# Kernel tuning notes

Measured on AMD Instinct MI355X. Metric: run time of the kernel, lower is better.

Reference implementation:

```python
import jax, jax.numpy as jnp
import numpy as np

NEG_SLOPE = 0.2  # PyG GATConv default negative_slope
EPS = 1e-16      # PyG softmax denominator epsilon


def setup_inputs() -> dict:
    key = jax.random.key(0)
    N, C, H, E = 50000, 64, 12, 400000
    k = jax.random.split(key, 5)
    x = jax.random.normal(k[0], (N, C), dtype=jnp.float32)
    edge_index = jax.random.randint(k[1], (2, E), 0, N, dtype=jnp.int32)
    W = jax.random.normal(k[2], (C, H * C), dtype=jnp.float32) * (1.0 / np.sqrt(C))
    att_src = jax.random.normal(k[3], (H, C), dtype=jnp.float32) * 0.1
    att_dst = jax.random.normal(k[4], (H, C), dtype=jnp.float32) * 0.1
    bias = jnp.zeros((C,), dtype=jnp.float32)
    return {"x": x, "edge_index": edge_index, "W": W,
            "att_src": att_src, "att_dst": att_dst, "bias": bias}


def reference(x, edge_index, W, att_src, att_dst, bias):
    N, C = x.shape
    H = att_src.shape[0]
    # GATConv default add_self_loops=True
    loops = jnp.arange(N, dtype=edge_index.dtype)
    src = jnp.concatenate([edge_index[0], loops])  # message source j
    dst = jnp.concatenate([edge_index[1], loops])  # message target i

    h = (x @ W).reshape(N, H, C)                   # [N,H,C] projected features
    a_src = jnp.einsum('nhc,hc->nh', h, att_src)   # [N,H]
    a_dst = jnp.einsum('nhc,hc->nh', h, att_dst)   # [N,H]

    alpha = jax.nn.leaky_relu(a_src[src] + a_dst[dst], NEG_SLOPE)  # [E',H]
    # segment softmax over destination neighborhoods
    m = jax.ops.segment_max(alpha, dst, num_segments=N)
    alpha = jnp.exp(alpha - m[dst])
    denom = jax.ops.segment_sum(alpha, dst, num_segments=N)
    alpha = alpha / (denom[dst] + EPS)

    msg = h[src] * alpha[:, :, None]               # [E',H,C]
    out = jax.ops.segment_sum(msg, dst, num_segments=N)  # [N,H,C]
    y = out.mean(axis=1) + bias                    # concat=False -> head mean
    return jax.nn.relu(x + y)
```

## Files before the change

### kernel.cpp

```cpp
#include <hip/hip_runtime.h>
#include <hip/hip_bf16.h>


typedef __bf16 bf16x8 __attribute__((ext_vector_type(8)));
typedef float  f32x4  __attribute__((ext_vector_type(4)));
typedef float  f32x2  __attribute__((ext_vector_type(2)));

#define HEADS 12
#define CH 64
#define HC 768
#define CAP 64
#define ACOLS 24
#define ZSTRIDE 776

__device__ inline float readlane_f(float v, int lane) {
    return __builtin_bit_cast(float,
        __builtin_amdgcn_readlane(__builtin_bit_cast(int, v), lane));
}

__global__ __launch_bounds__(256) void k_pre(
    const float* __restrict__ W,
    const float* __restrict__ att_src, const float* __restrict__ att_dst,
    int* __restrict__ cnt, __bf16* __restrict__ Wt2, __bf16* __restrict__ Vt,
    int N) {
    const int nb_z = (N + 255) >> 8;
    const int nb_w = (CH * HC) >> 8;
    int b = blockIdx.x, tid = threadIdx.x;
    if (b < nb_z) {
        int i = b * 256 + tid;
        if (i < N) cnt[i] = 0;
        return;
    }
    b -= nb_z;
    if (b < nb_w) {
        int t = b * 256 + tid;
        int c = t / HC, kk = t % HC;
        int k = kk & 63;
        Wt2[t] = (__bf16)W[(size_t)k * HC + (kk - k) + c];
        return;
    }
    b -= nb_w;
    if (b >= 2 * HEADS) {
        if (tid < CH) Vt[b * CH + tid] = (__bf16)0.f;
        return;
    }
    const float* att = (b < HEADS) ? att_src + b * CH
                                   : att_dst + (b - HEADS) * CH;
    int k = tid >> 2, cq = tid & 3;
    const float* wr = W + (size_t)k * HC + (b % HEADS) * CH + cq * 16;
    float s = 0.f;
#pragma unroll
    for (int j = 0; j < 16; ++j) s += wr[j] * att[cq * 16 + j];
    s += __shfl_xor(s, 1, 64);
    s += __shfl_xor(s, 2, 64);
    if (cq == 0) Vt[b * CH + k] = (__bf16)s;
}

__global__ __launch_bounds__(256) void k_main(
    const float* __restrict__ x, const int* __restrict__ ei,
    const __bf16* __restrict__ Vt,
    int* __restrict__ cnt, int* __restrict__ adj,
    __bf16* __restrict__ xb, float* __restrict__ a_all, int N, int E) {
    const int EP = E + N;
    const int nb_build = (EP + 255) >> 8;
    int b = blockIdx.x, tid = threadIdx.x;

    if (b < nb_build) {
        int e = b * 256 + tid;
        if (e < EP) {
            int d, s;
            if (e < E) { d = ei[E + e]; s = ei[e]; }
            else       { d = e - E;     s = d; }
            int pos = atomicAdd(&cnt[d], 1);
            if (pos < CAP) adj[d * CAP + pos] = s;
        }
        return;
    }
    b -= nb_build;
    int wave = tid >> 6, lane = tid & 63;
    int m = lane & 15, quad = lane >> 4;
    int m0 = b * 64 + wave * 16;
    int row = m0 + m;
    int rc = row < N ? row : N - 1;
    const float* xa = x + (size_t)rc * CH + quad * 8;
    f32x4 v0 = *(const f32x4*)xa;
    f32x4 v1 = *(const f32x4*)(xa + 4);
    f32x4 v2 = *(const f32x4*)(xa + 32);
    f32x4 v3 = *(const f32x4*)(xa + 36);
    bf16x8 a0, a1;
#pragma unroll
    for (int j = 0; j < 4; ++j) {
        a0[j] = (__bf16)v0[j]; a0[4 + j] = (__bf16)v1[j];
        a1[j] = (__bf16)v2[j]; a1[4 + j] = (__bf16)v3[j];
    }
    if (row < N) {
        *(bf16x8*)(xb + (size_t)row * CH + quad * 8) = a0;
        *(bf16x8*)(xb + (size_t)row * CH + quad * 8 + 32) = a1;
    }
#pragma unroll
    for (int t = 0; t < 2; ++t) {
        const __bf16* bp = Vt + (size_t)(t * 16 + m) * CH + quad * 8;
        bf16x8 b0 = *(const bf16x8*)bp;
        bf16x8 b1 = *(const bf16x8*)(bp + 32);
        f32x4 acc = {0.f, 0.f, 0.f, 0.f};
        acc = __builtin_amdgcn_mfma_f32_16x16x32_bf16(a0, b0, acc, 0, 0, 0);
        acc = __builtin_amdgcn_mfma_f32_16x16x32_bf16(a1, b1, acc, 0, 0, 0);
        int col = t * 16 + m;
        if (col < ACOLS) {
#pragma unroll
            for (int r = 0; r < 4; ++r) {
                int rr = m0 + quad * 4 + r;
                if (rr < N) a_all[(size_t)rr * ACOLS + col] = acc[r];
            }
        }
    }
}

__global__ __launch_bounds__(256) void k_fused(
    const int* __restrict__ cnt, const int* __restrict__ adj,
    const float* __restrict__ a_all,
    const __bf16* __restrict__ xb, const __bf16* __restrict__ Wt2,
    const float* __restrict__ x, const float* __restrict__ bias,
    float* __restrict__ out, int N) {
    __shared__ __bf16 zt[16 * ZSTRIDE];
    int lane = threadIdx.x & 63;
    int wave = __builtin_amdgcn_readfirstlane(threadIdx.x >> 6);
    int base = blockIdx.x * 16;

    int degj[4], slj[4];
#pragma unroll
    for (int j = 0; j < 4; ++j) {
        int d = base + wave * 4 + j;
        int dg = __builtin_amdgcn_readfirstlane(cnt[d]);
        degj[j] = dg < CAP ? dg : CAP;
        int sraw = 0;
        if (lane < 32) sraw = adj[d * CAP + lane];
        slj[j] = sraw;
    }

#pragma unroll
    for (int j = 0; j < 4; ++j) {
        int row = wave * 4 + j;
        int d = base + row;
        int deg = degj[j];
        int s_l = slj[j];
        if (deg > 32 && lane >= 32)
            s_l = adj[d * CAP + lane];
        s_l = s_l < 0 ? 0 : (s_l >= N ? N - 1 : s_l);

        float adf[HEADS];
        {
            const f32x4* p = (const f32x4*)(a_all + (size_t)d * ACOLS + HEADS);
            f32x4 t0 = p[0], t1 = p[1], t2 = p[2];
#pragma unroll
            for (int u = 0; u < 4; ++u) { adf[u] = t0[u]; adf[4 + u] = t1[u]; adf[8 + u] = t2[u]; }
        }
        float w[HEADS];
        {
            const f32x4* p = (const f32x4*)(a_all + (size_t)s_l * ACOLS);
            f32x4 t0 = p[0], t1 = p[1], t2 = p[2];
            float asf[HEADS];
#pragma unroll
            for (int u = 0; u < 4; ++u) { asf[u] = t0[u]; asf[4 + u] = t1[u]; asf[8 + u] = t2[u]; }
#pragma unroll
            for (int hh = 0; hh < HEADS; ++hh) {
                float sc = asf[hh] + adf[hh];
                sc = sc > 0.f ? sc : 0.2f * sc;
                w[hh] = __expf(sc);
            }
        }

        f32x2 acc2[HEADS];
#pragma unroll
        for (int hh = 0; hh < HEADS; ++hh) acc2[hh] = (f32x2){0.f, 0.f};
        int i = 0;
        for (; i + 3 < deg; i += 4) {
            int s0 = __builtin_amdgcn_readlane(s_l, i);
            int s1 = __builtin_amdgcn_readlane(s_l, i + 1);
            int s2 = __builtin_amdgcn_readlane(s_l, i + 2);
            int s3 = __builtin_amdgcn_readlane(s_l, i + 3);
            f32x2 xv0 = {(float)xb[(size_t)s0 * CH + lane], 1.f};
            f32x2 xv1 = {(float)xb[(size_t)s1 * CH + lane], 1.f};
            f32x2 xv2 = {(float)xb[(size_t)s2 * CH + lane], 1.f};
            f32x2 xv3 = {(float)xb[(size_t)s3 * CH + lane], 1.f};
#pragma unroll
            for (int hh = 0; hh < HEADS; ++hh) {
                float w0 = readlane_f(w[hh], i);
                float w1 = readlane_f(w[hh], i + 1);
                float w2 = readlane_f(w[hh], i + 2);
                float w3 = readlane_f(w[hh], i + 3);
                acc2[hh] += (f32x2){w0, w0} * xv0;
                acc2[hh] += (f32x2){w1, w1} * xv1;
                acc2[hh] += (f32x2){w2, w2} * xv2;
                acc2[hh] += (f32x2){w3, w3} * xv3;
            }
        }
        for (; i < deg; ++i) {
            int s = __builtin_amdgcn_readlane(s_l, i);
            f32x2 xv = {(float)xb[(size_t)s * CH + lane], 1.f};
#pragma unroll
            for (int hh = 0; hh < HEADS; ++hh) {
                float wv = readlane_f(w[hh], i);
                acc2[hh] += (f32x2){wv, wv} * xv;
            }
        }
        __bf16* zr = zt + row * ZSTRIDE + lane;
#pragma unroll
        for (int hh = 0; hh < HEADS; ++hh)
            zr[hh * CH] = (__bf16)(acc2[hh].x * (1.0f / ((acc2[hh].y + 1e-16f) * HEADS)));
    }

    __syncthreads();

    {
        int m = lane & 15, quad = lane >> 4;
        int n0 = wave * 16;
        const __bf16* za = zt + m * ZSTRIDE + quad * 8;
        const __bf16* wb = Wt2 + (size_t)(n0 + m) * HC + quad * 8;
        f32x4 acc = {0.f, 0.f, 0.f, 0.f};
#pragma unroll
        for (int kc = 0; kc < HC; kc += 32) {
            bf16x8 a  = *(const bf16x8*)(za + kc);
            bf16x8 bf = *(const bf16x8*)(wb + kc);
            acc = __builtin_amdgcn_mfma_f32_16x16x32_bf16(a, bf, acc, 0, 0, 0);
        }
        int col = n0 + m;
        float bv = bias[col];
#pragma unroll
        for (int r = 0; r < 4; ++r) {
            int dd = base + quad * 4 + r;
            if (dd < N) {
                float o = x[(size_t)dd * CH + col] + acc[r] + bv;
                out[(size_t)dd * CH + col] = fmaxf(o, 0.f);
            }
        }
    }
}

extern "C" void kernel_launch(void* const* d_in, const int* in_sizes, int n_in,
                              void* d_out, int out_size, void* d_ws, size_t ws_size,
                              hipStream_t stream) {
    const float* x       = (const float*)d_in[0];
    const int*   ei      = (const int*)d_in[1];
    const float* W       = (const float*)d_in[2];
    const float* att_src = (const float*)d_in[3];
    const float* att_dst = (const float*)d_in[4];
    const float* bias    = (const float*)d_in[5];
    float* out = (float*)d_out;

    int N = in_sizes[0] / CH;
    int E = in_sizes[1] / 2;
    int EP = E + N;

    char* ws = (char*)d_ws;
    size_t off = 0;
    auto take = [&](size_t bytes) -> void* {
        void* p = ws + off;
        off = (off + bytes + 255) & ~(size_t)255;
        return p;
    };
    __bf16* xb    = (__bf16*)take((size_t)N * CH * sizeof(__bf16));
    __bf16* Wt2   = (__bf16*)take((size_t)CH * HC * sizeof(__bf16));
    __bf16* Vt    = (__bf16*)take((size_t)32 * CH * sizeof(__bf16));
    float*  a_all = (float*)take((size_t)N * ACOLS * sizeof(float));
    int*    adj   = (int*)take((size_t)N * CAP * sizeof(int));
    int*    cnt   = (int*)take((size_t)N * sizeof(int));

    const int nb_z     = (N + 255) / 256;
    const int nb_w     = (CH * HC) / 256;
    const int nb_build = (EP + 255) / 256;
    const int nb_ax    = (N + 63) / 64;

    k_pre<<<nb_z + nb_w + 32, 256, 0, stream>>>(W, att_src, att_dst, cnt, Wt2, Vt, N);
    k_main<<<nb_build + nb_ax, 256, 0, stream>>>(x, ei, Vt, cnt, adj, xb, a_all, N, E);
    k_fused<<<(N + 15) / 16, 256, 0, stream>>>(cnt, adj, a_all, xb, Wt2, x, bias, out, N);
}
```

Before: 175.4 us.

## Replace scalar per-head neighbor aggregation with MFMA over LDS-staged neighbor features

The per-destination weighted sum over neighbors for all 12 heads becomes a bf16 MFMA. Gathered neighbor features go into a swizzled per-wave LDS tile and the attention weights into a small LDS matrix. A second MFMA against a ones vector computes the softmax denominator, and the z tile layout changes to a padded per-head stride. This removes the many readlane and VALU FMA operations per neighbor, at the cost of rounding the attention weights to bf16, extra LDS traffic and a fixed 32-neighbor MFMA per pass regardless of degree.

```diff
diff --git a/kernel.cpp b/kernel.cpp
--- a/kernel.cpp
+++ b/kernel.cpp
@@ -3,20 +3,19 @@
 
 
 typedef __bf16 bf16x8 __attribute__((ext_vector_type(8)));
+typedef __bf16 bf16x2 __attribute__((ext_vector_type(2)));
 typedef float  f32x4  __attribute__((ext_vector_type(4)));
-typedef float  f32x2  __attribute__((ext_vector_type(2)));
 
 #define HEADS 12
 #define CH 64
 #define HC 768
 #define CAP 64
 #define ACOLS 24
-#define ZSTRIDE 776
-
-__device__ inline float readlane_f(float v, int lane) {
-    return __builtin_bit_cast(float,
-        __builtin_amdgcn_readlane(__builtin_bit_cast(int, v), lane));
-}
+#define ZST 872
+#define HST 72
+#define XST 40
+#define WST 40
+#define XSW(c, i) ((c) * XST + ((i) ^ ((((c) >> 2) & 3) << 3)))
 
 __global__ __launch_bounds__(256) void k_pre(
     const float* __restrict__ W,
@@ -122,10 +121,24 @@
     const __bf16* __restrict__ xb, const __bf16* __restrict__ Wt2,
     const float* __restrict__ x, const float* __restrict__ bias,
     float* __restrict__ out, int N) {
-    __shared__ __bf16 zt[16 * ZSTRIDE];
+    __shared__ __bf16 zt[16 * ZST];
+    __shared__ __bf16 xs_all[4][CH * XST];
+    __shared__ __bf16 wl_all[4][16 * WST];
     int lane = threadIdx.x & 63;
     int wave = __builtin_amdgcn_readfirstlane(threadIdx.x >> 6);
     int base = blockIdx.x * 16;
+    __bf16* xs = xs_all[wave];
+    __bf16* wl = wl_all[wave];
+
+    {
+        unsigned* xz = (unsigned*)(xs + lane * XST);
+#pragma unroll
+        for (int t = 0; t < 16; ++t) xz[t] = 0u;
+    }
+
+    bf16x8 ones;
+#pragma unroll
+    for (int jj = 0; jj < 8; ++jj) ones[jj] = (__bf16)1.0f;
 
     int degj[4], slj[4];
 #pragma unroll
@@ -135,79 +148,124 @@
         degj[j] = dg < CAP ? dg : CAP;
         int sraw = 0;
         if (lane < 32) sraw = adj[d * CAP + lane];
-        slj[j] = sraw;
-    }
+        slj[j] = sraw < 0 ? 0 : (sraw >= N ? N - 1 : sraw);
+    }
+
+    const unsigned short* xbu = (const unsigned short*)xb;
 
 #pragma unroll
     for (int j = 0; j < 4; ++j) {
-        int row = wave * 4 + j;
-        int d = base + row;
+        int nodeRow = wave * 4 + j;
+        int d = base + nodeRow;
         int deg = degj[j];
-        int s_l = slj[j];
-        if (deg > 32 && lane >= 32)
-            s_l = adj[d * CAP + lane];
-        s_l = s_l < 0 ? 0 : (s_l >= N ? N - 1 : s_l);
 
         float adf[HEADS];
         {
             const f32x4* p = (const f32x4*)(a_all + (size_t)d * ACOLS + HEADS);
-            f32x4 t0 = p[0], t1 = p[1], t2 = p[2];
-#pragma unroll
-            for (int u = 0; u < 4; ++u) { adf[u] = t0[u]; adf[4 + u] = t1[u]; adf[8 + u] = t2[u]; }
-        }
-        float w[HEADS];
-        {
-            const f32x4* p = (const f32x4*)(a_all + (size_t)s_l * ACOLS);
-            f32x4 t0 = p[0], t1 = p[1], t2 = p[2];
-            float asf[HEADS];
-#pragma unroll
-            for (int u = 0; u < 4; ++u) { asf[u] = t0[u]; asf[4 + u] = t1[u]; asf[8 + u] = t2[u]; }
+            f32x4 q0 = p[0], q1 = p[1], q2 = p[2];
+#pragma unroll
+            for (int u = 0; u < 4; ++u) { adf[u] = q0[u]; adf[4 + u] = q1[u]; adf[8 + u] = q2[u]; }
+        }
+
+        f32x4 acc0 = {0.f,0.f,0.f,0.f}, acc1 = {0.f,0.f,0.f,0.f};
+        f32x4 acc2 = {0.f,0.f,0.f,0.f}, acc3 = {0.f,0.f,0.f,0.f};
+        f32x4 accden = {0.f,0.f,0.f,0.f};
+
+        auto do_pass = [&](int s_ll, int dc) {
+            f32x4 t0 = {0.f,0.f,0.f,0.f}, t1 = {0.f,0.f,0.f,0.f}, t2 = {0.f,0.f,0.f,0.f};
+            if (lane < dc) {
+                const f32x4* p = (const f32x4*)(a_all + (size_t)s_ll * ACOLS);
+                t0 = p[0]; t1 = p[1]; t2 = p[2];
+            }
+            float wv[HEADS];
+#pragma unroll
+            for (int u = 0; u < 4; ++u) {
+                wv[u]     = t0[u] + adf[u];
+                wv[4 + u] = t1[u] + adf[4 + u];
+                wv[8 + u] = t2[u] + adf[8 + u];
+            }
 #pragma unroll
             for (int hh = 0; hh < HEADS; ++hh) {
-                float sc = asf[hh] + adf[hh];
+                float sc = wv[hh];
                 sc = sc > 0.f ? sc : 0.2f * sc;
-                w[hh] = __expf(sc);
-            }
-        }
-
-        f32x2 acc2[HEADS];
-#pragma unroll
-        for (int hh = 0; hh < HEADS; ++hh) acc2[hh] = (f32x2){0.f, 0.f};
-        int i = 0;
-        for (; i + 3 < deg; i += 4) {
-            int s0 = __builtin_amdgcn_readlane(s_l, i);
-            int s1 = __builtin_amdgcn_readlane(s_l, i + 1);
-            int s2 = __builtin_amdgcn_readlane(s_l, i + 2);
-            int s3 = __builtin_amdgcn_readlane(s_l, i + 3);
-            f32x2 xv0 = {(float)xb[(size_t)s0 * CH + lane], 1.f};
-            f32x2 xv1 = {(float)xb[(size_t)s1 * CH + lane], 1.f};
-            f32x2 xv2 = {(float)xb[(size_t)s2 * CH + lane], 1.f};
-            f32x2 xv3 = {(float)xb[(size_t)s3 * CH + lane], 1.f};
-#pragma unroll
-            for (int hh = 0; hh < HEADS; ++hh) {
-                float w0 = readlane_f(w[hh], i);
-                float w1 = readlane_f(w[hh], i + 1);
-                float w2 = readlane_f(w[hh], i + 2);
-                float w3 = readlane_f(w[hh], i + 3);
-                acc2[hh] += (f32x2){w0, w0} * xv0;
-                acc2[hh] += (f32x2){w1, w1} * xv1;
-                acc2[hh] += (f32x2){w2, w2} * xv2;
-                acc2[hh] += (f32x2){w3, w3} * xv3;
-            }
-        }
-        for (; i < deg; ++i) {
-            int s = __builtin_amdgcn_readlane(s_l, i);
-            f32x2 xv = {(float)xb[(size_t)s * CH + lane], 1.f};
-#pragma unroll
-            for (int hh = 0; hh < HEADS; ++hh) {
-                float wv = readlane_f(w[hh], i);
-                acc2[hh] += (f32x2){wv, wv} * xv;
-            }
-        }
-        __bf16* zr = zt + row * ZSTRIDE + lane;
-#pragma unroll
-        for (int hh = 0; hh < HEADS; ++hh)
-            zr[hh * CH] = (__bf16)(acc2[hh].x * (1.0f / ((acc2[hh].y + 1e-16f) * HEADS)));
+                wv[hh] = (lane < dc) ? __expf(sc) : 0.f;
+            }
+            if (lane < 32) {
+#pragma unroll
+                for (int hh = 0; hh < HEADS; ++hh)
+                    wl[hh * WST + lane] = (__bf16)wv[hh];
+            }
+            int i = 0;
+            for (; i + 3 < dc; i += 4) {
+                int s0 = __builtin_amdgcn_readlane(s_ll, i);
+                int s1 = __builtin_amdgcn_readlane(s_ll, i + 1);
+                int s2 = __builtin_amdgcn_readlane(s_ll, i + 2);
+                int s3 = __builtin_amdgcn_readlane(s_ll, i + 3);
+                unsigned u0 = xbu[(size_t)s0 * CH + lane];
+                unsigned u1 = xbu[(size_t)s1 * CH + lane];
+                unsigned u2 = xbu[(size_t)s2 * CH + lane];
+                unsigned u3 = xbu[(size_t)s3 * CH + lane];
+                unsigned* dst = (unsigned*)(xs + XSW(lane, i));
+                dst[0] = u0 | (u1 << 16);
+                dst[1] = u2 | (u3 << 16);
+            }
+            for (; i < dc; ++i) {
+                int s = __builtin_amdgcn_readlane(s_ll, i);
+                xs[XSW(lane, i)] = xb[(size_t)s * CH + lane];
+            }
+            int hq = lane & 15, q = lane >> 4;
+            bf16x8 bfrag = *(const bf16x8*)(wl + hq * WST + q * 8);
+            {
+                int row = hq;
+                bf16x8 a = *(const bf16x8*)(xs + row * XST + ((q * 8) ^ (((row >> 2) & 3) << 3)));
+                acc0 = __builtin_amdgcn_mfma_f32_16x16x32_bf16(a, bfrag, acc0, 0, 0, 0);
+            }
+            {
+                int row = 16 + hq;
+                bf16x8 a = *(const bf16x8*)(xs + row * XST + ((q * 8) ^ (((row >> 2) & 3) << 3)));
+                acc1 = __builtin_amdgcn_mfma_f32_16x16x32_bf16(a, bfrag, acc1, 0, 0, 0);
+            }
+            {
+                int row = 32 + hq;
+                bf16x8 a = *(const bf16x8*)(xs + row * XST + ((q * 8) ^ (((row >> 2) & 3) << 3)));
+                acc2 = __builtin_amdgcn_mfma_f32_16x16x32_bf16(a, bfrag, acc2, 0, 0, 0);
+            }
+            {
+                int row = 48 + hq;
+                bf16x8 a = *(const bf16x8*)(xs + row * XST + ((q * 8) ^ (((row >> 2) & 3) << 3)));
+                acc3 = __builtin_amdgcn_mfma_f32_16x16x32_bf16(a, bfrag, acc3, 0, 0, 0);
+            }
+            accden = __builtin_amdgcn_mfma_f32_16x16x32_bf16(ones, bfrag, accden, 0, 0, 0);
+        };
+
+        int dc0 = deg < 32 ? deg : 32;
+        do_pass(slj[j], dc0);
+        if (deg > 32) {
+            int s2 = 0;
+            if (lane < 32) {
+                s2 = adj[d * CAP + 32 + lane];
+                s2 = s2 < 0 ? 0 : (s2 >= N ? N - 1 : s2);
+            }
+            do_pass(s2, deg - 32);
+        }
+
+        float den = accden[0];
+        float rinv = 1.0f / ((den + 1e-16f) * (float)HEADS);
+        int h = lane & 15, q = lane >> 4;
+        if (h < HEADS) {
+            __bf16* zr = zt + nodeRow * ZST + h * HST + q * 4;
+            f32x4 av[4] = {acc0, acc1, acc2, acc3};
+#pragma unroll
+            for (int t = 0; t < 4; ++t) {
+                bf16x2 p0, p1;
+                p0[0] = (__bf16)(av[t][0] * rinv);
+                p0[1] = (__bf16)(av[t][1] * rinv);
+                p1[0] = (__bf16)(av[t][2] * rinv);
+                p1[1] = (__bf16)(av[t][3] * rinv);
+                *(bf16x2*)(zr + t * 16) = p0;
+                *(bf16x2*)(zr + t * 16 + 2) = p1;
+            }
+        }
     }
 
     __syncthreads();
@@ -215,12 +273,13 @@
     {
         int m = lane & 15, quad = lane >> 4;
         int n0 = wave * 16;
-        const __bf16* za = zt + m * ZSTRIDE + quad * 8;
+        const __bf16* za = zt + m * ZST + quad * 8;
         const __bf16* wb = Wt2 + (size_t)(n0 + m) * HC + quad * 8;
         f32x4 acc = {0.f, 0.f, 0.f, 0.f};
 #pragma unroll
         for (int kc = 0; kc < HC; kc += 32) {
-            bf16x8 a  = *(const bf16x8*)(za + kc);
+            int koff = ((kc >> 6) * HST) + (kc & 63);
+            bf16x8 a  = *(const bf16x8*)(za + koff);
             bf16x8 bf = *(const bf16x8*)(wb + kc);
             acc = __builtin_amdgcn_mfma_f32_16x16x32_bf16(a, bf, acc, 0, 0, 0);
         }
```

Measured after the change: 187.9 us. +7.1%, slower.

## Compute per-head neighbor aggregation with MFMA and double-buffer neighbor gathers

Applied to the files above, without the earlier changes.

The per-destination weighted sum over neighbors, previously done with scalar readlane broadcasts and per-head FMAs, now runs as 32x32x16 bf16 MFMAs. Attention weights are staged in LDS as the B operand, and gathered neighbor feature rows are packed into the A operand. Gathers and attention loads for the next destination node are issued before the current node is computed, a software double-buffer, and the z tile layout is restrided with a per-head padding. This cuts VALU and readlane overhead, but rounds the weights and denominators to bf16, which lowers accuracy, and it raises register and LDS use.

```diff
diff --git a/kernel.cpp b/kernel.cpp
--- a/kernel.cpp
+++ b/kernel.cpp
@@ -3,20 +3,19 @@
 
 
 typedef __bf16 bf16x8 __attribute__((ext_vector_type(8)));
+typedef __bf16 bf16x4v __attribute__((ext_vector_type(4)));
 typedef float  f32x4  __attribute__((ext_vector_type(4)));
-typedef float  f32x2  __attribute__((ext_vector_type(2)));
+typedef float  f32x16 __attribute__((ext_vector_type(16)));
+typedef unsigned u32x4 __attribute__((ext_vector_type(4)));
 
 #define HEADS 12
 #define CH 64
 #define HC 768
 #define CAP 64
 #define ACOLS 24
-#define ZSTRIDE 776
-
-__device__ inline float readlane_f(float v, int lane) {
-    return __builtin_bit_cast(float,
-        __builtin_amdgcn_readlane(__builtin_bit_cast(int, v), lane));
-}
+#define ZST 872
+#define HST 72
+#define WLST 24
 
 __global__ __launch_bounds__(256) void k_pre(
     const float* __restrict__ W,
@@ -122,12 +121,21 @@
     const __bf16* __restrict__ xb, const __bf16* __restrict__ Wt2,
     const float* __restrict__ x, const float* __restrict__ bias,
     float* __restrict__ out, int N) {
-    __shared__ __bf16 zt[16 * ZSTRIDE];
+    __shared__ __bf16 zt[16 * ZST];
+    __shared__ __bf16 wl_all[4][2][32 * WLST];
     int lane = threadIdx.x & 63;
     int wave = __builtin_amdgcn_readfirstlane(threadIdx.x >> 6);
     int base = blockIdx.x * 16;
-
-    int degj[4], slj[4];
+    int g = lane >> 5, m = lane & 31;
+    int ib4 = g * 32;
+
+    {
+        unsigned* wz = (unsigned*)&wl_all[wave][0][0];
+#pragma unroll
+        for (int t = 0; t < 12; ++t) wz[t * 64 + lane] = 0u;
+    }
+
+    int degj[4], slj[4], dcj[4];
 #pragma unroll
     for (int j = 0; j < 4; ++j) {
         int d = base + wave * 4 + j;
@@ -135,96 +143,194 @@
         degj[j] = dg < CAP ? dg : CAP;
         int sraw = 0;
         if (lane < 32) sraw = adj[d * CAP + lane];
-        slj[j] = sraw;
-    }
-
+        slj[j] = sraw < 0 ? 0 : (sraw >= N ? N - 1 : sraw);
+    }
+
+    const unsigned short* xbu = (const unsigned short*)xb;
+
+    f32x4 sg0[2], sg1[2], sg2[2];
+    unsigned sa0[2][8], sa1[2][8];
+    float adfs[2][HEADS];
+
+    auto issue = [&](int j, int buf) {
+        int d = base + wave * 4 + j;
+        int dc = degj[j] < 16 ? degj[j] : 16;
+        dcj[j] = dc;
+        const float* ap = a_all + (size_t)d * ACOLS + HEADS;
+#pragma unroll
+        for (int hh = 0; hh < HEADS; ++hh) adfs[buf][hh] = ap[hh];
+        f32x4 z4 = {0.f, 0.f, 0.f, 0.f};
+        sg0[buf] = z4; sg1[buf] = z4; sg2[buf] = z4;
+        if (lane < dc) {
+            const f32x4* p = (const f32x4*)(a_all + (size_t)slj[j] * ACOLS);
+            sg0[buf] = p[0]; sg1[buf] = p[1]; sg2[buf] = p[2];
+        }
+#pragma unroll
+        for (int j8 = 0; j8 < 8; ++j8) {
+            int srow = __builtin_amdgcn_ds_bpermute(ib4 + j8 * 4, slj[j]);
+            int slot = g * 8 + j8;
+            unsigned v0 = 0, v1 = 0;
+            if (slot < dc) {
+                size_t o = (size_t)srow * CH + m;
+                v0 = xbu[o];
+                v1 = xbu[o + 32];
+            }
+            sa0[buf][j8] = v0;
+            sa1[buf][j8] = v1;
+        }
+    };
+
+    auto compute = [&](int j, int buf) {
+        int nodeRow = wave * 4 + j;
+        int d = base + nodeRow;
+        int dc = dcj[j];
+        int deg = degj[j];
+        __bf16* wl = &wl_all[wave][buf][0];
+
+        float wv[HEADS];
+        {
+            float asf[HEADS];
+#pragma unroll
+            for (int u = 0; u < 4; ++u) {
+                asf[u] = sg0[buf][u]; asf[4 + u] = sg1[buf][u]; asf[8 + u] = sg2[buf][u];
+            }
+#pragma unroll
+            for (int hh = 0; hh < HEADS; ++hh) {
+                float sc = asf[hh] + adfs[buf][hh];
+                sc = sc > 0.f ? sc : 0.2f * sc;
+                wv[hh] = (lane < dc) ? __expf(sc) : 0.f;
+            }
+        }
+        if (lane < 16) {
+#pragma unroll
+            for (int hh = 0; hh < HEADS; ++hh)
+                wl[hh * WLST + lane] = (__bf16)wv[hh];
+        }
+
+        bf16x8 bfrag = *(const bf16x8*)(wl + m * WLST + g * 8);
+        float den = 0.f;
+        {
+            bf16x8 d0 = *(const bf16x8*)(wl + m * WLST);
+            bf16x8 d1 = *(const bf16x8*)(wl + m * WLST + 8);
+#pragma unroll
+            for (int t = 0; t < 8; ++t) den += (float)d0[t] + (float)d1[t];
+        }
+
+        u32x4 p0, p1;
+#pragma unroll
+        for (int t = 0; t < 4; ++t) {
+            p0[t] = (sa0[buf][2 * t] & 0xffffu) | (sa0[buf][2 * t + 1] << 16);
+            p1[t] = (sa1[buf][2 * t] & 0xffffu) | (sa1[buf][2 * t + 1] << 16);
+        }
+        bf16x8 a0f = __builtin_bit_cast(bf16x8, p0);
+        bf16x8 a1f = __builtin_bit_cast(bf16x8, p1);
+
+        f32x16 acc0, acc1;
+#pragma unroll
+        for (int t = 0; t < 16; ++t) { acc0[t] = 0.f; acc1[t] = 0.f; }
+        acc0 = __builtin_amdgcn_mfma_f32_32x32x16_bf16(a0f, bfrag, acc0, 0, 0, 0);
+        acc1 = __builtin_amdgcn_mfma_f32_32x32x16_bf16(a1f, bfrag, acc1, 0, 0, 0);
+
+        if (deg > 16) {
+            int npass = (deg + 15) >> 4;
+            for (int p = 1; p < npass; ++p) {
+                int dcp = deg - 16 * p; if (dcp > 16) dcp = 16;
+                int sid = 0;
+                if (lane < 16) {
+                    int sr = adj[d * CAP + 16 * p + lane];
+                    sid = sr < 0 ? 0 : (sr >= N ? N - 1 : sr);
+                }
+                f32x4 q0 = {0.f,0.f,0.f,0.f}, q1 = q0, q2 = q0;
+                if (lane < dcp) {
+                    const f32x4* pp = (const f32x4*)(a_all + (size_t)sid * ACOLS);
+                    q0 = pp[0]; q1 = pp[1]; q2 = pp[2];
+                }
+                float wp[HEADS];
+#pragma unroll
+                for (int u = 0; u < 4; ++u) {
+                    wp[u]     = q0[u] + adfs[buf][u];
+                    wp[4 + u] = q1[u] + adfs[buf][4 + u];
+                    wp[8 + u] = q2[u] + adfs[buf][8 + u];
+                }
+#pragma unroll
+                for (int hh = 0; hh < HEADS; ++hh) {
+                    float sc = wp[hh];
+                    sc = sc > 0.f ? sc : 0.2f * sc;
+                    wp[hh] = (lane < dcp) ? __expf(sc) : 0.f;
+                }
+                if (lane < 16) {
+#pragma unroll
+                    for (int hh = 0; hh < HEADS; ++hh)
+                        wl[hh * WLST + lane] = (__bf16)wp[hh];
+                }
+                u32x4 r0, r1;
+#pragma unroll
+                for (int j8 = 0; j8 < 8; ++j8) {
+                    int srow = __builtin_amdgcn_ds_bpermute(ib4 + j8 * 4, sid);
+                    int slot = g * 8 + j8;
+                    unsigned v0 = 0, v1 = 0;
+                    if (slot < dcp) {
+                        size_t o = (size_t)srow * CH + m;
+                        v0 = xbu[o]; v1 = xbu[o + 32];
+                    }
+                    if (j8 & 1) { r0[j8 >> 1] |= v0 << 16; r1[j8 >> 1] |= v1 << 16; }
+                    else        { r0[j8 >> 1] = v0;        r1[j8 >> 1] = v1; }
+                }
+                bf16x8 bf2 = *(const bf16x8*)(wl + m * WLST + g * 8);
+                bf16x8 e0 = *(const bf16x8*)(wl + m * WLST);
+                bf16x8 e1 = *(const bf16x8*)(wl + m * WLST + 8);
+#pragma unroll
+                for (int t = 0; t < 8; ++t) den += (float)e0[t] + (float)e1[t];
+                acc0 = __builtin_amdgcn_mfma_f32_32x32x16_bf16(
+                    __builtin_bit_cast(bf16x8, r0), bf2, acc0, 0, 0, 0);
+                acc1 = __builtin_amdgcn_mfma_f32_32x32x16_bf16(
+                    __builtin_bit_cast(bf16x8, r1), bf2, acc1, 0, 0, 0);
+            }
+        }
+
+        float rinv = 1.0f / ((den + 1e-16f) * (float)HEADS);
+        if (m < HEADS) {
+            __bf16* zr = zt + nodeRow * ZST + m * HST;
+#pragma unroll
+            for (int ch = 0; ch < 2; ++ch) {
+#pragma unroll
+                for (int rr = 0; rr < 4; ++rr) {
+                    int c0 = 8 * rr + 4 * g + 32 * ch;
+                    bf16x4v pk;
+#pragma unroll
+                    for (int i = 0; i < 4; ++i) {
+                        float v = ch ? acc1[4 * rr + i] : acc0[4 * rr + i];
+                        pk[i] = (__bf16)(v * rinv);
+                    }
+                    *(bf16x4v*)(zr + c0) = pk;
+                }
+            }
+        }
+    };
+
+    issue(0, 0);
 #pragma unroll
     for (int j = 0; j < 4; ++j) {
-        int row = wave * 4 + j;
-        int d = base + row;
-        int deg = degj[j];
-        int s_l = slj[j];
-        if (deg > 32 && lane >= 32)
-            s_l = adj[d * CAP + lane];
-        s_l = s_l < 0 ? 0 : (s_l >= N ? N - 1 : s_l);
-
-        float adf[HEADS];
-        {
-            const f32x4* p = (const f32x4*)(a_all + (size_t)d * ACOLS + HEADS);
-            f32x4 t0 = p[0], t1 = p[1], t2 = p[2];
-#pragma unroll
-            for (int u = 0; u < 4; ++u) { adf[u] = t0[u]; adf[4 + u] = t1[u]; adf[8 + u] = t2[u]; }
-        }
-        float w[HEADS];
-        {
-            const f32x4* p = (const f32x4*)(a_all + (size_t)s_l * ACOLS);
-            f32x4 t0 = p[0], t1 = p[1], t2 = p[2];
-            float asf[HEADS];
-#pragma unroll
-            for (int u = 0; u < 4; ++u) { asf[u] = t0[u]; asf[4 + u] = t1[u]; asf[8 + u] = t2[u]; }
-#pragma unroll
-            for (int hh = 0; hh < HEADS; ++hh) {
-                float sc = asf[hh] + adf[hh];
-                sc = sc > 0.f ? sc : 0.2f * sc;
-                w[hh] = __expf(sc);
-            }
-        }
-
-        f32x2 acc2[HEADS];
-#pragma unroll
-        for (int hh = 0; hh < HEADS; ++hh) acc2[hh] = (f32x2){0.f, 0.f};
-        int i = 0;
-        for (; i + 3 < deg; i += 4) {
-            int s0 = __builtin_amdgcn_readlane(s_l, i);
-            int s1 = __builtin_amdgcn_readlane(s_l, i + 1);
-            int s2 = __builtin_amdgcn_readlane(s_l, i + 2);
-            int s3 = __builtin_amdgcn_readlane(s_l, i + 3);
-            f32x2 xv0 = {(float)xb[(size_t)s0 * CH + lane], 1.f};
-            f32x2 xv1 = {(float)xb[(size_t)s1 * CH + lane], 1.f};
-            f32x2 xv2 = {(float)xb[(size_t)s2 * CH + lane], 1.f};
-            f32x2 xv3 = {(float)xb[(size_t)s3 * CH + lane], 1.f};
-#pragma unroll
-            for (int hh = 0; hh < HEADS; ++hh) {
-                float w0 = readlane_f(w[hh], i);
-                float w1 = readlane_f(w[hh], i + 1);
-                float w2 = readlane_f(w[hh], i + 2);
-                float w3 = readlane_f(w[hh], i + 3);
-                acc2[hh] += (f32x2){w0, w0} * xv0;
-                acc2[hh] += (f32x2){w1, w1} * xv1;
-                acc2[hh] += (f32x2){w2, w2} * xv2;
-                acc2[hh] += (f32x2){w3, w3} * xv3;
-            }
-        }
-        for (; i < deg; ++i) {
-            int s = __builtin_amdgcn_readlane(s_l, i);
-            f32x2 xv = {(float)xb[(size_t)s * CH + lane], 1.f};
-#pragma unroll
-            for (int hh = 0; hh < HEADS; ++hh) {
-                float wv = readlane_f(w[hh], i);
-                acc2[hh] += (f32x2){wv, wv} * xv;
-            }
-        }
-        __bf16* zr = zt + row * ZSTRIDE + lane;
-#pragma unroll
-        for (int hh = 0; hh < HEADS; ++hh)
-            zr[hh * CH] = (__bf16)(acc2[hh].x * (1.0f / ((acc2[hh].y + 1e-16f) * HEADS)));
+        if (j < 3) issue(j + 1, (j + 1) & 1);
+        compute(j, j & 1);
     }
 
     __syncthreads();
 
     {
-        int m = lane & 15, quad = lane >> 4;
+        int mm = lane & 15, quad = lane >> 4;
         int n0 = wave * 16;
-        const __bf16* za = zt + m * ZSTRIDE + quad * 8;
-        const __bf16* wb = Wt2 + (size_t)(n0 + m) * HC + quad * 8;
+        const __bf16* za = zt + mm * ZST + quad * 8;
+        const __bf16* wb = Wt2 + (size_t)(n0 + mm) * HC + quad * 8;
         f32x4 acc = {0.f, 0.f, 0.f, 0.f};
 #pragma unroll
         for (int kc = 0; kc < HC; kc += 32) {
-            bf16x8 a  = *(const bf16x8*)(za + kc);
+            int koff = ((kc >> 6) * HST) + (kc & 63);
+            bf16x8 a  = *(const bf16x8*)(za + koff);
             bf16x8 bf = *(const bf16x8*)(wb + kc);
             acc = __builtin_amdgcn_mfma_f32_16x16x32_bf16(a, bf, acc, 0, 0, 0);
         }
-        int col = n0 + m;
+        int col = n0 + mm;
         float bv = bias[col];
 #pragma unroll
         for (int r = 0; r < 4; ++r) {
```

After: 194.8 us. 1.11x slower.
